# Kernel tuning notes

Measured on AMD Instinct MI355X. Metric: run time of the kernel, lower is better.

The kernel has to match this reference:

```python
import jax, jax.numpy as jnp
import numpy as np

N = 8192          # tokens
CD = 512          # coarse_dim
FD = 512          # fine_dim
CB = 4096         # coarse codebook size
FB = 8192         # fine codebook size
COST = 0.25       # commitment cost
LRELU = 0.1
EPS = 1e-5


def _vq(x, emb):
    # squared-distance cdist: [n, K]
    d = jnp.sum(x * x, axis=1, keepdims=True) + jnp.sum(emb * emb, axis=1) - 2.0 * (x @ emb.T)
    idx = jnp.argmin(d, axis=1)          # temperature=1.0 (updates=0); scaling doesn't change argmin
    q = emb[idx]                          # gather == one-hot @ emb, without materializing one-hot
    e_loss = jnp.mean((jax.lax.stop_gradient(q) - x) ** 2)
    q_loss = jnp.mean((q - jax.lax.stop_gradient(x)) ** 2)
    loss = q_loss + COST * e_loss
    q_st = x + jax.lax.stop_gradient(q - x)   # straight-through
    return q_st, loss


def _mlp(x, w, b, g, be):
    # Linear (torch: x @ W.T + b) -> LayerNorm -> LeakyReLU(0.1)
    h = x @ w.T + b
    m = jnp.mean(h, axis=-1, keepdims=True)
    v = jnp.var(h, axis=-1, keepdims=True)
    h = (h - m) / jnp.sqrt(v + EPS) * g + be
    return jnp.where(h > 0, h, LRELU * h)


def setup_inputs() -> dict:
    key = jax.random.key(0)
    ks = jax.random.split(key, 6)
    xav_c = float(np.sqrt(6.0 / (CB + CD)))
    xav_f = float(np.sqrt(6.0 / (FB + FD)))
    lin_s = float(np.sqrt(1.0 / CD))
    return {
        'z': jax.random.normal(ks[0], (N, CD + FD), dtype=jnp.float32),
        'coarse_emb': jax.random.uniform(ks[1], (CB, CD), jnp.float32, -xav_c, xav_c),
        'fine_emb': jax.random.uniform(ks[2], (FB, FD), jnp.float32, -xav_f, xav_f),
        'w_c2f': jax.random.uniform(ks[3], (FD, CD), jnp.float32, -lin_s, lin_s),
        'b_c2f': jnp.zeros((FD,), jnp.float32),
        'g_c2f': jnp.ones((FD,), jnp.float32),
        'be_c2f': jnp.zeros((FD,), jnp.float32),
        'w_f2c': jax.random.uniform(ks[4], (CD, FD), jnp.float32, -lin_s, lin_s),
        'b_f2c': jnp.zeros((CD,), jnp.float32),
        'g_f2c': jnp.ones((CD,), jnp.float32),
        'be_f2c': jnp.zeros((CD,), jnp.float32),
        'gate_c_raw': jnp.float32(0.5),
        'gate_f_raw': jnp.float32(0.5),
    }


def reference(z, coarse_emb, fine_emb, w_c2f, b_c2f, g_c2f, be_c2f,
              w_f2c, b_f2c, g_f2c, be_f2c, gate_c_raw, gate_f_raw):
    split = z.shape[1] // 2
    z_coarse, z_fine = z[:, :split], z[:, split:]

    z_coarse_q, coarse_loss = _vq(z_coarse, coarse_emb)
    coarse_influence = _mlp(jax.lax.stop_gradient(z_coarse_q), w_c2f, b_c2f, g_c2f, be_c2f)
    gate_c = jax.nn.sigmoid(gate_c_raw)

    residual = z_fine - gate_c * coarse_influence
    z_fine_q, fine_loss = _vq(residual, fine_emb)

    fine_feedback = _mlp(jax.lax.stop_gradient(z_fine_q), w_f2c, b_f2c, g_f2c, be_f2c)
    gate_f = jax.nn.sigmoid(gate_f_raw)

    z_coarse_corrected = z_coarse_q + 0.1 * gate_f * fine_feedback
    z_fine_reconstructed = z_fine_q + gate_c * coarse_influence
    z_hierarchical = jnp.concatenate([z_coarse_corrected, z_fine_reconstructed], axis=1)
    vq_loss = coarse_loss + fine_loss
    return z_hierarchical, vq_loss
```

## Files before the change

### kernel.cpp

```cpp
#include <hip/hip_runtime.h>
#include <hip/hip_bf16.h>
#include <cstdint>
#include <cstddef>

#define KD 512

#define OFF_CN   0u
#define OFF_FN   16384u
#define OFF_ZN   49152u
#define OFF_RN   81920u
#define OFF_LOSS 114688u
#define OFF_AMC  114944u
#define OFF_AMF  180480u
#define OFF_CEH  246016u
#define OFF_CEL  4440320u
#define OFF_FEH  8634624u
#define OFF_FEL  17023232u
#define OFF_ZCH  25411840u
#define OFF_ZCL  33800448u
#define OFF_RH   42189056u
#define OFF_RL   50577664u
#define OFF_W1H  58966272u
#define OFF_W1L  59490560u
#define OFF_W2H  60014848u
#define OFF_W2L  60539136u
#define OFF_H    61063424u
#define OFF_INFL 77840640u


typedef __attribute__((ext_vector_type(8))) short bf16x8;
typedef __attribute__((ext_vector_type(4))) float f32x4;
typedef unsigned long long u64;

__device__ __forceinline__ bf16x8 as_bf16x8(int4 v) {
  union { int4 i; bf16x8 b; } u; u.i = v; return u.b;
}

__device__ __forceinline__ void gl_lds16(const void* g, void* l) {
  __builtin_amdgcn_global_load_lds(
      (const __attribute__((address_space(1))) void*)g,
      (__attribute__((address_space(3))) void*)l, 16, 0, 0);
}

__device__ __forceinline__ float block_sum(float v, float* sred) {
#pragma unroll
  for (int off = 32; off > 0; off >>= 1) v += __shfl_down(v, off, 64);
  if ((threadIdx.x & 63) == 0) sred[threadIdx.x >> 6] = v;
  __syncthreads();
  float r = sred[0] + sred[1] + sred[2] + sred[3];
  __syncthreads();
  return r;
}

__device__ __forceinline__ float sigmoidf_(float x) { return 1.0f / (1.0f + expf(-x)); }

__device__ __forceinline__ void split_bf16(float v, __hip_bfloat16* hi, __hip_bfloat16* lo) {
  __hip_bfloat16 h = __float2bfloat16(v);
  *hi = h;
  *lo = __float2bfloat16(v - __bfloat162float(h));
}

__device__ __forceinline__ unsigned enc_sortable(float f) {
  unsigned u = __float_as_uint(f);
  return (u & 0x80000000u) ? ~u : (u | 0x80000000u);
}
__device__ __forceinline__ float dec_sortable(unsigned ub) {
  unsigned o = (ub & 0x80000000u) ? (ub & 0x7fffffffu) : ~ub;
  return __uint_as_float(o);
}
__device__ __forceinline__ u64 umin64(u64 a, u64 b) { return a < b ? a : b; }
__device__ __forceinline__ u64 umax64(u64 a, u64 b) { return a > b ? a : b; }

__device__ __forceinline__ void merge3(u64& a1, u64& a2, u64& a3, u64 b1, u64 b2, u64 b3) {
  u64 p = umax64(a1, b1);
  u64 q = umin64(a2, b2);
  u64 r = umax64(a2, b2);
  u64 s = umin64(a3, b3);
  u64 m1 = umin64(a1, b1);
  u64 m2 = umin64(p, q);
  u64 m3 = umin64(umin64(umax64(p, q), r), s);
  a1 = m1; a2 = m2; a3 = m3;
}

__global__ __launch_bounds__(256) void prep(
    const float* __restrict__ ce, const float* __restrict__ fe, const float* __restrict__ z,
    const float* __restrict__ w1, const float* __restrict__ w2,
    float* __restrict__ cn, float* __restrict__ fn, float* __restrict__ zn,
    __hip_bfloat16* __restrict__ ceH, __hip_bfloat16* __restrict__ ceL,
    __hip_bfloat16* __restrict__ feH, __hip_bfloat16* __restrict__ feL,
    __hip_bfloat16* __restrict__ zcH,
    __hip_bfloat16* __restrict__ w1H, __hip_bfloat16* __restrict__ w1L,
    __hip_bfloat16* __restrict__ w2H, __hip_bfloat16* __restrict__ w2L,
    float* __restrict__ lossp) {
  __shared__ float sred[4];
  const int b = blockIdx.x, t = threadIdx.x;
  const float* src;
  float* nd = nullptr;
  __hip_bfloat16 *dh = nullptr, *dl = nullptr;
  int fragMode = 0, hiOnly = 0;
  size_t row;
  if (b < 4096) {
    row = b; src = ce + row * KD; nd = cn + row; dh = ceH; dl = ceL; fragMode = 1;
  } else if (b < 12288) {
    row = b - 4096; src = fe + row * KD; nd = fn + row; dh = feH; dl = feL; fragMode = 1;
  } else if (b < 20480) {
    row = b - 12288; src = z + row * 1024; nd = zn + row; dh = zcH; hiOnly = 1;
  } else if (b < 20992) {
    row = b - 20480; src = w1 + row * KD; dh = w1H; dl = w1L;
  } else {
    row = b - 20992; src = w2 + row * KD; dh = w2H; dl = w2L;
  }
  float acc = 0.0f;
  if (fragMode) {
    float v0 = src[t], v1 = src[t + 256];
    acc = v0 * v0 + v1 * v1;
  } else {
#pragma unroll
    for (int j = 0; j < 2; ++j) {
      int c = t + j * 256;
      float v = src[c];
      acc += v * v;
      __hip_bfloat16 h, l;
      split_bf16(v, &h, &l);
      dh[row * KD + c] = h;
      if (!hiOnly) dl[row * KD + c] = l;
    }
  }
  if (nd) {
    float s = block_sum(acc, sred);
    if (t == 0) nd[0] = s;
  } else {
    __syncthreads();
    __syncthreads();
  }
  if (fragMode && t < 64) {
    union { int4 i; __hip_bfloat16 s[8]; } ph, pl;
#pragma unroll
    for (int j = 0; j < 8; ++j) {
      float v = src[8 * t + j];
      split_bf16(v, &ph.s[j], &pl.s[j]);
    }
    const int chunkIdx = (int)(((row >> 4) * 16 + (t >> 2)) * 64 +
                               ((size_t)((t & 3) << 4) | (row & 15)));
    ((int4*)dh)[chunkIdx] = ph.i;
    ((int4*)dl)[chunkIdx] = pl.i;
  }
  if (b == 20480 && t == 0) lossp[0] = 0.0f;
}

__global__ __launch_bounds__(256) void vq9(
    const int4* __restrict__ AfH,
    const __hip_bfloat16* __restrict__ Bh,
    const float* __restrict__ cn,
    u64* __restrict__ bkeys) {
  __shared__ __align__(16) int4 sA[3][512];
  __shared__ __align__(16) __hip_bfloat16 sB[3][128 * 32];
  const int t = threadIdx.x;
  const int w = t >> 6, l = t & 63;

  const int bx = blockIdx.x;
  const int by = blockIdx.y;
  const int rowTile = by << 7;
  const int colTile = bx << 7;
  const int NB = gridDim.y;
  const int wr = (w >> 1) << 6;
  const int wc = (w & 1) << 6;

  const int rl = l >> 2;
  const int sbp = (l & 3) ^ ((l >> 3) & 3);
  const size_t gOff0 = (size_t)(colTile + (w << 5) + rl) * KD + (sbp << 3);
  const size_t gOff1 = gOff0 + (size_t)16 * KD;
  const int lOffB0 = (w << 5) << 5;
  const int lOffB1 = lOffB0 + (16 << 5);

  const int rtg = rowTile >> 4;
  const int aS0 = ((rtg + 2 * w) << 10) + l;
  const int aS1 = ((rtg + 2 * w + 1) << 10) + l;

  const int fr = l & 15;
  const int q = l >> 4;

  f32x4 acc[4][4];
#pragma unroll
  for (int i = 0; i < 4; ++i)
#pragma unroll
    for (int j = 0; j < 4; ++j) acc[i][j] = (f32x4){0.f, 0.f, 0.f, 0.f};

#define STAGE(ck) do {                                                   \
    const int sl_ = (ck) % 3;                                            \
    gl_lds16(AfH + aS0 + ((ck) << 6), &sA[sl_][(2 * w) << 6]);           \
    gl_lds16(AfH + aS1 + ((ck) << 6), &sA[sl_][(2 * w + 1) << 6]);       \
    gl_lds16(Bh + gOff0 + ((size_t)(ck) << 5), &sB[sl_][lOffB0]);        \
    gl_lds16(Bh + gOff1 + ((size_t)(ck) << 5), &sB[sl_][lOffB1]);        \
  } while (0)

  STAGE(0);
  STAGE(1);
  __builtin_amdgcn_sched_barrier(0);

#pragma unroll
  for (int i = 0; i < 16; ++i) {
    if (i < 15) asm volatile("s_waitcnt vmcnt(4) lgkmcnt(0)" ::: "memory");
    else        asm volatile("s_waitcnt vmcnt(0) lgkmcnt(0)" ::: "memory");
    __builtin_amdgcn_s_barrier();
    __builtin_amdgcn_sched_barrier(0);
    if (i + 2 < 16) STAGE(i + 2);
    __builtin_amdgcn_sched_barrier(0);

    const int cb = i % 3;
    bf16x8 afh[4], bfh[4];
#pragma unroll
    for (int mt = 0; mt < 4; ++mt)
      afh[mt] = as_bf16x8(sA[cb][(((w >> 1) << 2) + mt) * 64 + l]);
#pragma unroll
    for (int nt = 0; nt < 4; ++nt) {
      const int rB = wc + (nt << 4) + fr;
      const int o = (rB << 5) + ((q ^ ((rB >> 1) & 3)) << 3);
      bfh[nt] = *(const bf16x8*)(sB[cb] + o);
    }
    __builtin_amdgcn_s_setprio(1);
#pragma unroll
    for (int mt = 0; mt < 4; ++mt)
#pragma unroll
      for (int nt = 0; nt < 4; ++nt)
        acc[mt][nt] = __builtin_amdgcn_mfma_f32_16x16x32_bf16(afh[mt], bfh[nt], acc[mt][nt], 0, 0, 0);
    __builtin_amdgcn_s_setprio(0);
  }
#undef STAGE

  u64 tk1[4], tk2[4], tk3[4];
#pragma unroll
  for (int nt = 0; nt < 4; ++nt) {
    u64 t1 = ~0ULL, t2 = ~0ULL, t3 = ~0ULL;
#pragma unroll
    for (int mt = 0; mt < 4; ++mt) {
#pragma unroll
      for (int reg = 0; reg < 4; ++reg) {
        const int code = rowTile + wr + (mt << 4) + (q << 2) + reg;
        float d = cn[code] - 2.0f * acc[mt][nt][reg];
        u64 key = ((u64)enc_sortable(d) << 32) | (u64)(unsigned)code;
        if (key < t1) { t3 = t2; t2 = t1; t1 = key; }
        else if (key < t2) { t3 = t2; t2 = key; }
        else if (key < t3) { t3 = key; }
      }
    }
#pragma unroll
    for (int off = 16; off <= 32; off <<= 1) {
      u64 b1 = __shfl_xor(t1, off, 64);
      u64 b2 = __shfl_xor(t2, off, 64);
      u64 b3 = __shfl_xor(t3, off, 64);
      merge3(t1, t2, t3, b1, b2, b3);
    }
    tk1[nt] = t1; tk2[nt] = t2; tk3[nt] = t3;
  }

  __syncthreads();
  u64* sk = (u64*)sA;
  if (w >= 2 && l < 16) {
#pragma unroll
    for (int nt = 0; nt < 4; ++nt) {
      const int o = ((((w & 1) << 2) + nt) * 16 + fr) * 3;
      sk[o] = tk1[nt]; sk[o + 1] = tk2[nt]; sk[o + 2] = tk3[nt];
    }
  }
  __syncthreads();
  if (w < 2 && l < 16) {
#pragma unroll
    for (int nt = 0; nt < 4; ++nt) {
      const int o = (((w << 2) + nt) * 16 + fr) * 3;
      u64 t1 = tk1[nt], t2 = tk2[nt], t3 = tk3[nt];
      merge3(t1, t2, t3, sk[o], sk[o + 1], sk[o + 2]);
      const int query = colTile + wc + (nt << 4) + fr;
      const size_t bo = ((size_t)query * NB + by) * 3;
      bkeys[bo] = t1; bkeys[bo + 1] = t2; bkeys[bo + 2] = t3;
    }
  }
}

__global__ __launch_bounds__(256) void rescue(
    const u64* __restrict__ bkeys, int NB3,
    const float* __restrict__ Q, int qStride,
    const float* __restrict__ Cb,
    const float* __restrict__ qn, const float* __restrict__ cnorm,
    float dscale, u64* __restrict__ am) {
  const int wv = threadIdx.x >> 6, l = threadIdx.x & 63;
  const int qi = (blockIdx.x << 2) + wv;
  const u64* kq = bkeys + (size_t)qi * NB3;
  u64 kk[3];
#pragma unroll
  for (int j = 0; j < 3; ++j) {
    const int idx = l + (j << 6);
    kk[j] = (idx < NB3) ? kq[idx] : ~0ULL;
  }
  u64 kmin = umin64(kk[0], umin64(kk[1], kk[2]));
#pragma unroll
  for (int off = 32; off > 0; off >>= 1) kmin = umin64(kmin, __shfl_xor(kmin, off, 64));
  const float xnv = qn[qi];
  const float dmin = dec_sortable((unsigned)(kmin >> 32));
  const float thr = dmin + dscale * sqrtf(xnv) + 0.01f;
  const u64 thrKey = ((u64)enc_sortable(thr) << 32) | 0xffffffffULL;

  const float* qrow = Q + (size_t)qi * qStride;
  const float4 qa = *(const float4*)(qrow + (l << 3));
  const float4 qb = *(const float4*)(qrow + (l << 3) + 4);
  float bestD = 3.4e38f;
  int bestC = 0x7fffffff;
#pragma unroll
  for (int j = 0; j < 3; ++j) {
    bool pend = kk[j] <= thrKey;
    u64 mask;
    while ((mask = __ballot(pend)) != 0ULL) {
      const int src = __ffsll((unsigned long long)mask) - 1;
      const u64 key = __shfl(kk[j], src, 64);
      if (l == src) pend = false;
      const int code = (int)(unsigned)(key & 0xffffffffULL);
      const float* crow = Cb + (size_t)code * KD;
      const float4 ca = *(const float4*)(crow + (l << 3));
      const float4 cb = *(const float4*)(crow + (l << 3) + 4);
      float dt = qa.x * ca.x + qa.y * ca.y + qa.z * ca.z + qa.w * ca.w +
                 qb.x * cb.x + qb.y * cb.y + qb.z * cb.z + qb.w * cb.w;
#pragma unroll
      for (int off = 32; off > 0; off >>= 1) dt += __shfl_xor(dt, off, 64);
      const float d = (xnv + cnorm[code]) - 2.0f * dt;
      if (d < bestD || (d == bestD && code < bestC)) { bestD = d; bestC = code; }
    }
  }
  if (l == 0) am[qi] = ((u64)enc_sortable(bestD) << 32) | (unsigned)bestC;
}

__global__ __launch_bounds__(256) void mlp6(
    const int4* __restrict__ AfH, const int4* __restrict__ AfL,
    const u64* __restrict__ gather,
    const __hip_bfloat16* __restrict__ Bh, const __hip_bfloat16* __restrict__ Bl,
    const float* __restrict__ bias, float* __restrict__ C) {
  __shared__ __align__(16) __hip_bfloat16 sAh[128 * 32];
  __shared__ __align__(16) __hip_bfloat16 sAl[128 * 32];
  __shared__ __align__(16) __hip_bfloat16 sBh[128 * 32];
  __shared__ __align__(16) __hip_bfloat16 sBl[128 * 32];
  const int t = threadIdx.x;
  const int w = t >> 6, l = t & 63;
  const int rowTile = blockIdx.y << 7;
  const int colTile = blockIdx.x << 7;
  const int wr = (w >> 1) << 6;
  const int wc = (w & 1) << 6;

  const int srow = t >> 2;
  const int sb = t & 3;
  const int skE = sb << 3;
  const int swz = (sb ^ ((srow >> 1) & 3)) << 3;
  const int wOff0 = (srow << 5) + swz;
  const int wOff1 = ((srow + 64) << 5) + swz;

  unsigned i0 = ((const unsigned*)gather)[2 * (rowTile + srow)];
  unsigned i1 = ((const unsigned*)gather)[2 * (rowTile + 64 + srow)];
  const int a0 = (int)((i0 >> 4) << 10) + (sb << 4) + (int)(i0 & 15);
  const int a1 = (int)((i1 >> 4) << 10) + (sb << 4) + (int)(i1 & 15);
  const size_t br0 = (size_t)(colTile + srow) * KD;
  const size_t br1 = (size_t)(colTile + 64 + srow) * KD;

  const int fr = l & 15;
  const int q = l >> 4;

  f32x4 acc[4][4];
#pragma unroll
  for (int i = 0; i < 4; ++i)
#pragma unroll
    for (int j = 0; j < 4; ++j) acc[i][j] = (f32x4){0.f, 0.f, 0.f, 0.f};

  for (int kk = 0; kk < KD; kk += 32) {
    const int kc64 = (kk >> 5) << 6;
    int4 vAh0 = AfH[a0 + kc64];
    int4 vAh1 = AfH[a1 + kc64];
    int4 vAl0 = AfL[a0 + kc64];
    int4 vAl1 = AfL[a1 + kc64];
    int4 vBh0 = *(const int4*)(Bh + br0 + kk + skE);
    int4 vBh1 = *(const int4*)(Bh + br1 + kk + skE);
    int4 vBl0 = *(const int4*)(Bl + br0 + kk + skE);
    int4 vBl1 = *(const int4*)(Bl + br1 + kk + skE);
    __syncthreads();
    *(int4*)(sAh + wOff0) = vAh0; *(int4*)(sAh + wOff1) = vAh1;
    *(int4*)(sAl + wOff0) = vAl0; *(int4*)(sAl + wOff1) = vAl1;
    *(int4*)(sBh + wOff0) = vBh0; *(int4*)(sBh + wOff1) = vBh1;
    *(int4*)(sBl + wOff0) = vBl0; *(int4*)(sBl + wOff1) = vBl1;
    __syncthreads();

    bf16x8 afh[4], afl[4], bfh[4], bfl[4];
#pragma unroll
    for (int mt = 0; mt < 4; ++mt) {
      const int rA = wr + (mt << 4) + fr;
      const int o = (rA << 5) + ((q ^ ((rA >> 1) & 3)) << 3);
      afh[mt] = *(const bf16x8*)(sAh + o);
      afl[mt] = *(const bf16x8*)(sAl + o);
    }
#pragma unroll
    for (int nt = 0; nt < 4; ++nt) {
      const int rB = wc + (nt << 4) + fr;
      const int o = (rB << 5) + ((q ^ ((rB >> 1) & 3)) << 3);
      bfh[nt] = *(const bf16x8*)(sBh + o);
      bfl[nt] = *(const bf16x8*)(sBl + o);
    }
#pragma unroll
    for (int mt = 0; mt < 4; ++mt)
#pragma unroll
      for (int nt = 0; nt < 4; ++nt) {
        acc[mt][nt] = __builtin_amdgcn_mfma_f32_16x16x32_bf16(afh[mt], bfh[nt], acc[mt][nt], 0, 0, 0);
        acc[mt][nt] = __builtin_amdgcn_mfma_f32_16x16x32_bf16(afh[mt], bfl[nt], acc[mt][nt], 0, 0, 0);
        acc[mt][nt] = __builtin_amdgcn_mfma_f32_16x16x32_bf16(afl[mt], bfh[nt], acc[mt][nt], 0, 0, 0);
      }
  }

  const int quad = l >> 4;
#pragma unroll
  for (int mt = 0; mt < 4; ++mt) {
#pragma unroll
    for (int reg = 0; reg < 4; ++reg) {
      const int row = rowTile + wr + (mt << 4) + (quad << 2) + reg;
#pragma unroll
      for (int nt = 0; nt < 4; ++nt) {
        const int col = colTile + wc + (nt << 4) + fr;
        C[(size_t)row * KD + col] = acc[mt][nt][reg] + bias[col];
      }
    }
  }
}

__global__ __launch_bounds__(256) void ln_residual(
    const float* __restrict__ h, const float* __restrict__ g, const float* __restrict__ be,
    const float* __restrict__ z, const float* __restrict__ gRaw,
    __hip_bfloat16* __restrict__ infl, float* __restrict__ rn,
    __hip_bfloat16* __restrict__ rH, float* __restrict__ resF) {
  __shared__ float sred[4];
  const int row = blockIdx.x, t = threadIdx.x;
  const size_t base = (size_t)row * KD;
  float h0 = h[base + t], h1 = h[base + t + 256];
  float m = block_sum(h0 + h1, sred) * (1.0f / 512.0f);
  float d0 = h0 - m, d1 = h1 - m;
  float var = block_sum(d0 * d0 + d1 * d1, sred) * (1.0f / 512.0f);
  float sq = sqrtf(var + 1e-5f);
  float gc = sigmoidf_(gRaw[0]);
  float v0 = d0 / sq * g[t] + be[t];
  float v1 = d1 / sq * g[t + 256] + be[t + 256];
  v0 = v0 > 0.0f ? v0 : 0.1f * v0;
  v1 = v1 > 0.0f ? v1 : 0.1f * v1;
  infl[base + t] = __float2bfloat16(v0);
  infl[base + t + 256] = __float2bfloat16(v1);
  float zf0 = z[(size_t)row * 1024 + 512 + t];
  float zf1 = z[(size_t)row * 1024 + 512 + t + 256];
  float r0 = zf0 - gc * v0, r1 = zf1 - gc * v1;
  rH[base + t] = __float2bfloat16(r0);
  rH[base + t + 256] = __float2bfloat16(r1);
  resF[base + t] = r0;
  resF[base + t + 256] = r1;
  float rs = block_sum(r0 * r0 + r1 * r1, sred);
  if (t == 0) rn[row] = rs;
}

__global__ __launch_bounds__(256) void finalize(
    const float* __restrict__ h, const float* __restrict__ g, const float* __restrict__ be,
    const __hip_bfloat16* __restrict__ infl,
    const u64* __restrict__ amc, const u64* __restrict__ amf,
    const float* __restrict__ z, const float* __restrict__ ce, const float* __restrict__ fe,
    const float* __restrict__ gcRaw, const float* __restrict__ gfRaw,
    float* __restrict__ out, float* __restrict__ lossp) {
  __shared__ float sred[4];
  const int row = blockIdx.x, t = threadIdx.x;
  const size_t base = (size_t)row * KD;
  float h0 = h[base + t], h1 = h[base + t + 256];
  float m = block_sum(h0 + h1, sred) * (1.0f / 512.0f);
  float d0 = h0 - m, d1 = h1 - m;
  float var = block_sum(d0 * d0 + d1 * d1, sred) * (1.0f / 512.0f);
  float sq = sqrtf(var + 1e-5f);
  float fb0 = d0 / sq * g[t] + be[t];
  float fb1 = d1 / sq * g[t + 256] + be[t + 256];
  fb0 = fb0 > 0.0f ? fb0 : 0.1f * fb0;
  fb1 = fb1 > 0.0f ? fb1 : 0.1f * fb1;
  float gc = sigmoidf_(gcRaw[0]);
  float gf = sigmoidf_(gfRaw[0]);
  unsigned ic = (unsigned)(amc[row] & 0xffffffffULL);
  unsigned ifx = (unsigned)(amf[row] & 0xffffffffULL);
  float loc = 0.0f;
#pragma unroll
  for (int j = 0; j < 2; ++j) {
    int c = t + j * 256;
    float fb = j ? fb1 : fb0;
    float qc = ce[(size_t)ic * KD + c];
    float qf = fe[(size_t)ifx * KD + c];
    float zc = z[(size_t)row * 1024 + c];
    float zf = z[(size_t)row * 1024 + 512 + c];
    float fl = __bfloat162float(infl[base + c]);
    out[(size_t)row * 1024 + c] = qc + 0.1f * gf * fb;
    out[(size_t)row * 1024 + 512 + c] = qf + gc * fl;
    float dc = qc - zc;
    float res = zf - gc * fl;
    float df = qf - res;
    loc += dc * dc + df * df;
  }
  float ls = block_sum(loc, sred);
  if (t == 0) atomicAdd(lossp, ls);
}

__global__ void loss_write(const float* __restrict__ lossp, float* __restrict__ out) {
  out[0] = 1.25f * lossp[0] / (8192.0f * 512.0f);
}

extern "C" void kernel_launch(void* const* d_in, const int* in_sizes, int n_in,
                              void* d_out, int out_size, void* d_ws, size_t ws_size,
                              hipStream_t stream) {
  const float* z      = (const float*)d_in[0];
  const float* ce     = (const float*)d_in[1];
  const float* fe     = (const float*)d_in[2];
  const float* w_c2f  = (const float*)d_in[3];
  const float* b_c2f  = (const float*)d_in[4];
  const float* g_c2f  = (const float*)d_in[5];
  const float* be_c2f = (const float*)d_in[6];
  const float* w_f2c  = (const float*)d_in[7];
  const float* b_f2c  = (const float*)d_in[8];
  const float* g_f2c  = (const float*)d_in[9];
  const float* be_f2c = (const float*)d_in[10];
  const float* gcRaw  = (const float*)d_in[11];
  const float* gfRaw  = (const float*)d_in[12];
  float* out = (float*)d_out;
  char* ws = (char*)d_ws;

  float* cn = (float*)(ws + OFF_CN);
  float* fn = (float*)(ws + OFF_FN);
  float* zn = (float*)(ws + OFF_ZN);
  float* rn = (float*)(ws + OFF_RN);
  float* lossp = (float*)(ws + OFF_LOSS);
  u64* amc = (u64*)(ws + OFF_AMC);
  u64* amf = (u64*)(ws + OFF_AMF);
  __hip_bfloat16* ceH = (__hip_bfloat16*)(ws + OFF_CEH);
  __hip_bfloat16* ceL = (__hip_bfloat16*)(ws + OFF_CEL);
  __hip_bfloat16* feH = (__hip_bfloat16*)(ws + OFF_FEH);
  __hip_bfloat16* feL = (__hip_bfloat16*)(ws + OFF_FEL);
  __hip_bfloat16* zcH = (__hip_bfloat16*)(ws + OFF_ZCH);
  __hip_bfloat16* rH  = (__hip_bfloat16*)(ws + OFF_RH);
  __hip_bfloat16* w1H = (__hip_bfloat16*)(ws + OFF_W1H);
  __hip_bfloat16* w1L = (__hip_bfloat16*)(ws + OFF_W1L);
  __hip_bfloat16* w2H = (__hip_bfloat16*)(ws + OFF_W2H);
  __hip_bfloat16* w2L = (__hip_bfloat16*)(ws + OFF_W2L);
  float* h = (float*)(ws + OFF_H);
  __hip_bfloat16* infl = (__hip_bfloat16*)(ws + OFF_INFL);
  u64* bkeys = (u64*)(ws + OFF_H);
  float* resF = (float*)(ws + OFF_ZCH);

  prep<<<21504, 256, 0, stream>>>(ce, fe, z, w_c2f, w_f2c, cn, fn, zn,
                                  ceH, ceL, feH, feL, zcH,
                                  w1H, w1L, w2H, w2L, lossp);

  vq9<<<dim3(64, 32), 256, 0, stream>>>((const int4*)ceH, zcH, cn, bkeys);

  rescue<<<2048, 256, 0, stream>>>(bkeys, 96, z, 1024, ce, zn, cn, 0.00321f, amc);

  mlp6<<<dim3(4, 64), 256, 0, stream>>>((const int4*)ceH, (const int4*)ceL, amc,
                                        w1H, w1L, b_c2f, h);

  ln_residual<<<8192, 256, 0, stream>>>(h, g_c2f, be_c2f, z, gcRaw, infl, rn, rH, resF);

  vq9<<<dim3(64, 64), 256, 0, stream>>>((const int4*)feH, rH, fn, bkeys);

  rescue<<<2048, 256, 0, stream>>>(bkeys, 192, resF, 512, fe, rn, fn, 0.00233f, amf);

  mlp6<<<dim3(4, 64), 256, 0, stream>>>((const int4*)feH, (const int4*)feL, amf,
                                        w2H, w2L, b_f2c, h);

  finalize<<<8192, 256, 0, stream>>>(h, g_f2c, be_f2c, infl, amc, amf, z, ce, fe,
                                     gcRaw, gfRaw, out, lossp);
  loss_write<<<1, 1, 0, stream>>>(lossp, out + (size_t)8192 * 1024);
}
```

Before: 576.7 us.

## Enlarge VQ distance tile to 256 codes by 128 queries per block

The VQ distance GEMM kernel now covers 256 codebook rows per block instead of 128. Each wave owns 64 codes across all 128 queries, so it holds 4x8 accumulators and reads all eight B fragments. This doubles reuse of each staged query tile and halves the number of per-block top-3 candidates the rescue kernel has to merge. The cost is more accumulator registers (launch bounds now request 2 blocks per SM), more LDS for the A tile, and a serial cross-wave merge done by wave 0.

```diff
diff --git a/kernel.cpp b/kernel.cpp
--- a/kernel.cpp
+++ b/kernel.cpp
@@ -148,23 +148,21 @@
   if (b == 20480 && t == 0) lossp[0] = 0.0f;
 }
 
-__global__ __launch_bounds__(256) void vq9(
+__global__ __launch_bounds__(256, 2) void vq10(
     const int4* __restrict__ AfH,
     const __hip_bfloat16* __restrict__ Bh,
     const float* __restrict__ cn,
     u64* __restrict__ bkeys) {
-  __shared__ __align__(16) int4 sA[3][512];
+  __shared__ __align__(16) int4 sA[3][1024];
   __shared__ __align__(16) __hip_bfloat16 sB[3][128 * 32];
   const int t = threadIdx.x;
   const int w = t >> 6, l = t & 63;
 
   const int bx = blockIdx.x;
   const int by = blockIdx.y;
-  const int rowTile = by << 7;
+  const int rowTile = by << 8;
   const int colTile = bx << 7;
   const int NB = gridDim.y;
-  const int wr = (w >> 1) << 6;
-  const int wc = (w & 1) << 6;
 
   const int rl = l >> 2;
   const int sbp = (l & 3) ^ ((l >> 3) & 3);
@@ -174,22 +172,26 @@
   const int lOffB1 = lOffB0 + (16 << 5);
 
   const int rtg = rowTile >> 4;
-  const int aS0 = ((rtg + 2 * w) << 10) + l;
-  const int aS1 = ((rtg + 2 * w + 1) << 10) + l;
+  const int aS0 = ((rtg + 4 * w + 0) << 10) + l;
+  const int aS1 = ((rtg + 4 * w + 1) << 10) + l;
+  const int aS2 = ((rtg + 4 * w + 2) << 10) + l;
+  const int aS3 = ((rtg + 4 * w + 3) << 10) + l;
 
   const int fr = l & 15;
   const int q = l >> 4;
 
-  f32x4 acc[4][4];
+  f32x4 acc[4][8];
 #pragma unroll
   for (int i = 0; i < 4; ++i)
 #pragma unroll
-    for (int j = 0; j < 4; ++j) acc[i][j] = (f32x4){0.f, 0.f, 0.f, 0.f};
+    for (int j = 0; j < 8; ++j) acc[i][j] = (f32x4){0.f, 0.f, 0.f, 0.f};
 
 #define STAGE(ck) do {                                                   \
     const int sl_ = (ck) % 3;                                            \
-    gl_lds16(AfH + aS0 + ((ck) << 6), &sA[sl_][(2 * w) << 6]);           \
-    gl_lds16(AfH + aS1 + ((ck) << 6), &sA[sl_][(2 * w + 1) << 6]);       \
+    gl_lds16(AfH + aS0 + ((ck) << 6), &sA[sl_][(4 * w + 0) << 6]);       \
+    gl_lds16(AfH + aS1 + ((ck) << 6), &sA[sl_][(4 * w + 1) << 6]);       \
+    gl_lds16(AfH + aS2 + ((ck) << 6), &sA[sl_][(4 * w + 2) << 6]);       \
+    gl_lds16(AfH + aS3 + ((ck) << 6), &sA[sl_][(4 * w + 3) << 6]);       \
     gl_lds16(Bh + gOff0 + ((size_t)(ck) << 5), &sB[sl_][lOffB0]);        \
     gl_lds16(Bh + gOff1 + ((size_t)(ck) << 5), &sB[sl_][lOffB1]);        \
   } while (0)
@@ -200,7 +202,7 @@
 
 #pragma unroll
   for (int i = 0; i < 16; ++i) {
-    if (i < 15) asm volatile("s_waitcnt vmcnt(4) lgkmcnt(0)" ::: "memory");
+    if (i < 15) asm volatile("s_waitcnt vmcnt(6) lgkmcnt(0)" ::: "memory");
     else        asm volatile("s_waitcnt vmcnt(0) lgkmcnt(0)" ::: "memory");
     __builtin_amdgcn_s_barrier();
     __builtin_amdgcn_sched_barrier(0);
@@ -208,13 +210,13 @@
     __builtin_amdgcn_sched_barrier(0);
 
     const int cb = i % 3;
-    bf16x8 afh[4], bfh[4];
+    bf16x8 afh[4], bfh[8];
 #pragma unroll
     for (int mt = 0; mt < 4; ++mt)
-      afh[mt] = as_bf16x8(sA[cb][(((w >> 1) << 2) + mt) * 64 + l]);
-#pragma unroll
-    for (int nt = 0; nt < 4; ++nt) {
-      const int rB = wc + (nt << 4) + fr;
+      afh[mt] = as_bf16x8(sA[cb][((4 * w) + mt) * 64 + l]);
+#pragma unroll
+    for (int nt = 0; nt < 8; ++nt) {
+      const int rB = (nt << 4) + fr;
       const int o = (rB << 5) + ((q ^ ((rB >> 1) & 3)) << 3);
       bfh[nt] = *(const bf16x8*)(sB[cb] + o);
     }
@@ -222,21 +224,21 @@
 #pragma unroll
     for (int mt = 0; mt < 4; ++mt)
 #pragma unroll
-      for (int nt = 0; nt < 4; ++nt)
+      for (int nt = 0; nt < 8; ++nt)
         acc[mt][nt] = __builtin_amdgcn_mfma_f32_16x16x32_bf16(afh[mt], bfh[nt], acc[mt][nt], 0, 0, 0);
     __builtin_amdgcn_s_setprio(0);
   }
 #undef STAGE
 
-  u64 tk1[4], tk2[4], tk3[4];
-#pragma unroll
-  for (int nt = 0; nt < 4; ++nt) {
+  u64 tk1[8], tk2[8], tk3[8];
+#pragma unroll
+  for (int nt = 0; nt < 8; ++nt) {
     u64 t1 = ~0ULL, t2 = ~0ULL, t3 = ~0ULL;
 #pragma unroll
     for (int mt = 0; mt < 4; ++mt) {
 #pragma unroll
       for (int reg = 0; reg < 4; ++reg) {
-        const int code = rowTile + wr + (mt << 4) + (q << 2) + reg;
+        const int code = rowTile + (w << 6) + (mt << 4) + (q << 2) + reg;
         float d = cn[code] - 2.0f * acc[mt][nt][reg];
         u64 key = ((u64)enc_sortable(d) << 32) | (u64)(unsigned)code;
         if (key < t1) { t3 = t2; t2 = t1; t1 = key; }
@@ -256,21 +258,24 @@
 
   __syncthreads();
   u64* sk = (u64*)sA;
-  if (w >= 2 && l < 16) {
-#pragma unroll
-    for (int nt = 0; nt < 4; ++nt) {
-      const int o = ((((w & 1) << 2) + nt) * 16 + fr) * 3;
+  if (w > 0 && l < 16) {
+#pragma unroll
+    for (int nt = 0; nt < 8; ++nt) {
+      const int o = (((w << 3) + nt) * 16 + fr) * 3;
       sk[o] = tk1[nt]; sk[o + 1] = tk2[nt]; sk[o + 2] = tk3[nt];
     }
   }
   __syncthreads();
-  if (w < 2 && l < 16) {
-#pragma unroll
-    for (int nt = 0; nt < 4; ++nt) {
-      const int o = (((w << 2) + nt) * 16 + fr) * 3;
+  if (w == 0 && l < 16) {
+#pragma unroll
+    for (int nt = 0; nt < 8; ++nt) {
       u64 t1 = tk1[nt], t2 = tk2[nt], t3 = tk3[nt];
-      merge3(t1, t2, t3, sk[o], sk[o + 1], sk[o + 2]);
-      const int query = colTile + wc + (nt << 4) + fr;
+#pragma unroll
+      for (int wv = 1; wv < 4; ++wv) {
+        const int o = (((wv << 3) + nt) * 16 + fr) * 3;
+        merge3(t1, t2, t3, sk[o], sk[o + 1], sk[o + 2]);
+      }
+      const int query = colTile + (nt << 4) + fr;
       const size_t bo = ((size_t)query * NB + by) * 3;
       bkeys[bo] = t1; bkeys[bo + 1] = t2; bkeys[bo + 2] = t3;
     }
@@ -548,18 +553,18 @@
                                   ceH, ceL, feH, feL, zcH,
                                   w1H, w1L, w2H, w2L, lossp);
 
-  vq9<<<dim3(64, 32), 256, 0, stream>>>((const int4*)ceH, zcH, cn, bkeys);
-
-  rescue<<<2048, 256, 0, stream>>>(bkeys, 96, z, 1024, ce, zn, cn, 0.00321f, amc);
+  vq10<<<dim3(64, 16), 256, 0, stream>>>((const int4*)ceH, zcH, cn, bkeys);
+
+  rescue<<<2048, 256, 0, stream>>>(bkeys, 48, z, 1024, ce, zn, cn, 0.00321f, amc);
 
   mlp6<<<dim3(4, 64), 256, 0, stream>>>((const int4*)ceH, (const int4*)ceL, amc,
                                         w1H, w1L, b_c2f, h);
 
   ln_residual<<<8192, 256, 0, stream>>>(h, g_c2f, be_c2f, z, gcRaw, infl, rn, rH, resF);
 
-  vq9<<<dim3(64, 64), 256, 0, stream>>>((const int4*)feH, rH, fn, bkeys);
-
-  rescue<<<2048, 256, 0, stream>>>(bkeys, 192, resF, 512, fe, rn, fn, 0.00233f, amf);
+  vq10<<<dim3(64, 32), 256, 0, stream>>>((const int4*)feH, rH, fn, bkeys);
+
+  rescue<<<2048, 256, 0, stream>>>(bkeys, 96, resF, 512, fe, rn, fn, 0.00233f, amf);
 
   mlp6<<<dim3(4, 64), 256, 0, stream>>>((const int4*)feH, (const int4*)feL, amf,
                                         w2H, w2L, b_f2c, h);
```

Measured after the change: 545.8 us. -5.4%, faster.
